# Optimization experiments

Measured on AMD Instinct MI355X. Metric: run time of the kernel, lower is better.

Reference implementation:

```python
import jax, jax.numpy as jnp
import numpy as np

EPS = 1e-5

def conv1x1(x, w):
    # x: (B,C,H,W), w: (O,C) -> (B,O,H,W)
    return jnp.einsum('bchw,oc->bohw', x, w)

def bn_relu(y, g, b, m, v):
    s = g / jnp.sqrt(v + EPS)
    return jax.nn.relu(y * s[None, :, None, None] + (b - m * s)[None, :, None, None])

def cbr(x, w, g, b, m, v):
    return bn_relu(conv1x1(x, w), g, b, m, v)

def _bn_params(key, c):
    k1, k2, k3, k4 = jax.random.split(key, 4)
    g = 1.0 + 0.1 * jax.random.normal(k1, (c,), jnp.float32)
    b = 0.1 * jax.random.normal(k2, (c,), jnp.float32)
    m = 0.05 * jax.random.normal(k3, (c,), jnp.float32)
    v = jax.random.uniform(k4, (c,), jnp.float32, 0.5, 1.5)
    return g, b, m, v

def setup_inputs() -> dict:
    key = jax.random.key(0)
    B, Cin, H, W = 8, 512, 64, 64
    Ck, Cv, Cout = 256, 256, 512
    ks = jax.random.split(key, 12)
    def w(k, o, c):
        return jax.random.normal(k, (o, c), jnp.float32) * (1.0 / np.sqrt(c))
    inp = {}
    inp['x'] = jax.random.normal(ks[0], (B, Cin, H, W), jnp.float32)
    # f_key
    inp['kW1'] = w(ks[1], Ck, Cin); inp['kG1'], inp['kB1'], inp['kM1'], inp['kV1'] = _bn_params(ks[2], Ck)
    inp['kW2'] = w(ks[3], Ck, Ck);  inp['kG2'], inp['kB2'], inp['kM2'], inp['kV2'] = _bn_params(ks[4], Ck)
    # f_query
    inp['qW1'] = w(ks[5], Ck, Cin); inp['qG1'], inp['qB1'], inp['qM1'], inp['qV1'] = _bn_params(ks[6], Ck)
    inp['qW2'] = w(ks[7], Ck, Ck);  inp['qG2'], inp['qB2'], inp['qM2'], inp['qV2'] = _bn_params(ks[8], Ck)
    # f_value
    inp['vW'] = w(ks[9], Cv, Cin)
    # W (output projection)
    inp['wW'] = w(ks[10], Cout, Cv); inp['wG'], inp['wB'], inp['wM'], inp['wV'] = _bn_params(ks[11], Cout)
    return inp

def reference(x,
              kW1, kG1, kB1, kM1, kV1, kW2, kG2, kB2, kM2, kV2,
              qW1, qG1, qB1, qM1, qV1, qW2, qG2, qB2, qM2, qV2,
              vW,
              wW, wG, wB, wM, wV):
    B, _, H, W = x.shape
    q = cbr(cbr(x, qW1, qG1, qB1, qM1, qV1), qW2, qG2, qB2, qM2, qV2)  # (B,Ck,H,W)
    k = cbr(cbr(x, kW1, kG1, kB1, kM1, kV1), kW2, kG2, kB2, kM2, kV2)  # (B,Ck,H,W)
    v = conv1x1(x, vW)                                                  # (B,Cv,H,W)
    Ck = q.shape[1]; Cv = v.shape[1]; N = H * W
    qf = q.reshape(B, Ck, N)   # query = qf^T -> (B,N,Ck)
    kf = k.reshape(B, Ck, N)
    vf = v.reshape(B, Cv, N)
    sim = jnp.einsum('bcn,bcm->bnm', qf, kf) * (Ck ** -0.5)  # (B,N,N)
    attn = jax.nn.softmax(sim, axis=-1)
    ctx = jnp.einsum('bnm,bcm->bcn', attn, vf).reshape(B, Cv, H, W)
    return cbr(ctx, wW, wG, wB, wM, wV)
```

## Files before the change

kernel.cpp:

```cpp
#include <hip/hip_runtime.h>
#include <hip/hip_bf16.h>

typedef __attribute__((ext_vector_type(8))) short bf16x8;
typedef __attribute__((ext_vector_type(4))) float f32x4;

#define MFMA16(a, b, c) __builtin_amdgcn_mfma_f32_16x16x32_bf16(a, b, c, 0, 0, 0)

static __device__ __forceinline__ unsigned short f2bf(float f) {
  union { __hip_bfloat16 h; unsigned short u; } cv;
  cv.h = __float2bfloat16(f);
  return cv.u;
}

static __device__ __forceinline__ void gload16(const void* gptr, void* lptr) {
  __builtin_amdgcn_global_load_lds(
      (const __attribute__((address_space(1))) void*)gptr,
      (__attribute__((address_space(3))) void*)lptr, 16, 0, 0);
}


__global__ void conv_w_k(const float* __restrict__ qW1, const float* __restrict__ kW1,
                         const float* __restrict__ qW2, const float* __restrict__ kW2,
                         const float* __restrict__ vW, const float* __restrict__ wW,
                         __hip_bfloat16* __restrict__ dst) {
  int i = blockIdx.x * 256 + threadIdx.x;
  const float* src; int off;
  if (i < 131072)      { src = qW1; off = i; }
  else if (i < 262144) { src = kW1; off = i - 131072; }
  else if (i < 327680) { src = qW2; off = i - 262144; }
  else if (i < 393216) { src = kW2; off = i - 327680; }
  else if (i < 524288) { src = vW;  off = i - 393216; }
  else                 { src = wW;  off = i - 524288; }
  dst[i] = __float2bfloat16(src[off]);
}

__global__ void bn_all_k(const float* __restrict__ qG1, const float* __restrict__ qB1, const float* __restrict__ qM1, const float* __restrict__ qV1,
                         const float* __restrict__ qG2, const float* __restrict__ qB2, const float* __restrict__ qM2, const float* __restrict__ qV2,
                         const float* __restrict__ kG1, const float* __restrict__ kB1, const float* __restrict__ kM1, const float* __restrict__ kV1,
                         const float* __restrict__ kG2, const float* __restrict__ kB2, const float* __restrict__ kM2, const float* __restrict__ kV2,
                         const float* __restrict__ wG, const float* __restrict__ wB, const float* __restrict__ wM, const float* __restrict__ wV,
                         float* __restrict__ base) {
  int bidx = blockIdx.x, tid = threadIdx.x;
  const float *g, *b, *m, *v; float *s, *t; int i;
  if (bidx == 0)      { g = qG1; b = qB1; m = qM1; v = qV1; s = base;        t = base + 256;  i = tid; }
  else if (bidx == 1) { g = qG2; b = qB2; m = qM2; v = qV2; s = base + 512;  t = base + 768;  i = tid; }
  else if (bidx == 2) { g = kG1; b = kB1; m = kM1; v = kV1; s = base + 1024; t = base + 1280; i = tid; }
  else if (bidx == 3) { g = kG2; b = kB2; m = kM2; v = kV2; s = base + 1536; t = base + 1792; i = tid; }
  else                { g = wG;  b = wB;  m = wM;  v = wV;  s = base + 2048; t = base + 2560; i = (bidx - 4) * 256 + tid; }
  float sv = g[i] * rsqrtf(v[i] + 1e-5f);
  s[i] = sv;
  t[i] = b[i] - m[i] * sv;
}

__global__ __launch_bounds__(256) void transpose_k(const float* __restrict__ x,
                                                   __hip_bfloat16* __restrict__ xT) {
  __shared__ float tile[64][65];
  const int n0 = blockIdx.x * 64, c0 = blockIdx.y * 64, b = blockIdx.z;
  const int tx = threadIdx.x, ty = threadIdx.y;
  const float* xp = x + ((size_t)(b * 512 + c0) * 4096) + n0;
#pragma unroll
  for (int i = 0; i < 16; ++i) {
    int c = ty + 4 * i;
    tile[c][tx] = xp[(size_t)c * 4096 + tx];
  }
  __syncthreads();
  __hip_bfloat16* op = xT + ((size_t)(b * 4096 + n0) * 512) + c0;
#pragma unroll
  for (int i = 0; i < 16; ++i) {
    int nl = ty + 4 * i;
    op[(size_t)nl * 512 + tx] = __float2bfloat16(tile[tx][nl]);
  }
}

template <int EPI>
__global__ __launch_bounds__(256) void gemm_nt_k(
    const __hip_bfloat16* __restrict__ A, long sA,
    const __hip_bfloat16* __restrict__ B, long sB,
    void* __restrict__ Cp, long sC,
    int lda, int ldb, int ldc, int K,
    const float* __restrict__ s, const float* __restrict__ t) {
  __shared__ short As[128][72];
  __shared__ short Bs[128][72];
  const int tid = threadIdx.x;
  const int w = tid >> 6, l = tid & 63, g = l >> 4, ln = l & 15;
  const int wr = w >> 1, wc = w & 1;
  const int rb = blockIdx.x * 128, cb = blockIdx.y * 128;
  const __hip_bfloat16* Ab = A + (size_t)blockIdx.z * sA;
  const __hip_bfloat16* Bb = B + (size_t)blockIdx.z * sB;

  f32x4 acc[4][4];
#pragma unroll
  for (int i = 0; i < 4; ++i)
#pragma unroll
    for (int j = 0; j < 4; ++j) acc[i][j] = (f32x4){0.f, 0.f, 0.f, 0.f};

  const int r0 = tid >> 3;
  const int c8 = (tid & 7) * 8;

  for (int k0 = 0; k0 < K; k0 += 64) {
#pragma unroll
    for (int i = 0; i < 4; ++i) {
      const int r = r0 + 32 * i;
      *(uint4*)&As[r][c8] = *(const uint4*)(Ab + (size_t)(rb + r) * lda + (k0 + c8));
      *(uint4*)&Bs[r][c8] = *(const uint4*)(Bb + (size_t)(cb + r) * ldb + (k0 + c8));
    }
    __syncthreads();
#pragma unroll
    for (int kk = 0; kk < 2; ++kk) {
      bf16x8 av[4], bv[4];
#pragma unroll
      for (int i = 0; i < 4; ++i) av[i] = *(const bf16x8*)&As[64 * wr + 16 * i + ln][32 * kk + 8 * g];
#pragma unroll
      for (int i = 0; i < 4; ++i) bv[i] = *(const bf16x8*)&Bs[64 * wc + 16 * i + ln][32 * kk + 8 * g];
#pragma unroll
      for (int mi = 0; mi < 4; ++mi)
#pragma unroll
        for (int ni = 0; ni < 4; ++ni)
          acc[mi][ni] = MFMA16(av[mi], bv[ni], acc[mi][ni]);
    }
    __syncthreads();
  }

  const int row0 = rb + 64 * wr + 4 * g;
  const int col0 = cb + 64 * wc + ln;

  if (EPI == 2) {
    float* C = (float*)Cp + (size_t)blockIdx.z * sC;
#pragma unroll
    for (int mi = 0; mi < 4; ++mi) {
#pragma unroll
      for (int r = 0; r < 4; ++r) {
        const int R = row0 + 16 * mi + r;
        const float sr = s[R], tr = t[R];
#pragma unroll
        for (int ni = 0; ni < 4; ++ni) {
          float v = fmaf(acc[mi][ni][r], sr, tr);
          C[(size_t)R * ldc + (col0 + 16 * ni)] = v > 0.f ? v : 0.f;
        }
      }
    }
  } else {
    __hip_bfloat16* C = (__hip_bfloat16*)Cp + (size_t)blockIdx.z * sC;
    float sc[4], tc[4];
    if (EPI == 1) {
#pragma unroll
      for (int ni = 0; ni < 4; ++ni) { sc[ni] = s[col0 + 16 * ni]; tc[ni] = t[col0 + 16 * ni]; }
    }
#pragma unroll
    for (int mi = 0; mi < 4; ++mi) {
#pragma unroll
      for (int ni = 0; ni < 4; ++ni) {
#pragma unroll
        for (int r = 0; r < 4; ++r) {
          float v = acc[mi][ni][r];
          if (EPI == 1) { v = fmaf(v, sc[ni], tc[ni]); v = v > 0.f ? v : 0.f; }
          C[(size_t)(row0 + 16 * mi + r) * ldc + (col0 + 16 * ni)] = __float2bfloat16(v);
        }
      }
    }
  }
}

__global__ __launch_bounds__(256, 2) void flash_k(
    const __hip_bfloat16* __restrict__ Q,
    const __hip_bfloat16* __restrict__ Kt,
    const __hip_bfloat16* __restrict__ V,
    __hip_bfloat16* __restrict__ O) {
  __shared__ short Ks[64 * 256];
  __shared__ short Ps[64 * 64];
  __shared__ float aLds[64];
  __shared__ float lLds[64];
  __shared__ int fLds[4];

  const int tid = threadIdx.x;
  const int w = tid >> 6, l = tid & 63, g = l >> 4, ln = l & 15;
  const int bid = blockIdx.x;
  const int batch = bid & 7;
  const int qb = (bid >> 3) << 6;
  const size_t bo = (size_t)batch * (4096 * 256);
  const float CE = 0.09016844005556021f;

  const int swz45 = (16 * g) ^ ((ln & 3) << 4);
  const int s6 = ((ln >> 2) & 1) << 6;
  const char* Ks0 = (const char*)Ks + (ln * 512 + swz45 + s6);
  const char* Ks1 = Ks0 + (((ln >> 2) & 1) ? -64 : 64);
  const char* Pr0 = (const char*)Ps + (ln * 128 + swz45 + s6);
  const char* Pr1 = Pr0 + (((ln >> 2) & 1) ? -64 : 64);
  const int pwOff = (16 * w + ln) * 128 + 8 * (g & 1) + (((g >> 1) ^ (ln & 1)) << 4) +
                    (((ln >> 1) & 1) << 5) + s6;

  bf16x8 qf[8];
  {
    const __hip_bfloat16* qp = Q + bo + (size_t)(qb + 16 * w + ln) * 256 + 8 * g;
#pragma unroll
    for (int kk = 0; kk < 8; ++kk) qf[kk] = *(const bf16x8*)(qp + 32 * kk);
  }

  f32x4 acc[4][4];
#pragma unroll
  for (int qg = 0; qg < 4; ++qg)
#pragma unroll
    for (int ci = 0; ci < 4; ++ci) acc[qg][ci] = (f32x4){0.f, 0.f, 0.f, 0.f};
  float m_run = -1e30f, l_run = 0.f;

  const int kRow = 16 * w + (l >> 5);
  const int kChunk = (l & 31) ^ (l >> 5);
  const short* Kb = (const short*)(Kt + bo);
  const short* Vp = (const short*)(V + bo) + (size_t)(64 * w + ln) * 4096 + 8 * g;

  auto stageK = [&](int m0) {
#pragma unroll
    for (int j = 0; j < 8; ++j) {
      const short* gp = Kb + (size_t)(m0 + kRow + 2 * j) * 256 + 8 * (kChunk ^ ((2 * j) & 7));
      gload16(gp, Ks + w * 4096 + j * 512);
    }
  };

  stageK(0);
  __builtin_amdgcn_sched_barrier(0);

  for (int t = 0; t < 64; ++t) {
    const int m0 = t << 6;

    bf16x8 vfr[8];
#pragma unroll
    for (int ci = 0; ci < 4; ++ci)
#pragma unroll
      for (int kk = 0; kk < 2; ++kk) {
        const short* gp = Vp + (size_t)ci * (16 * 4096) + (m0 + 32 * kk);
        asm volatile("global_load_dwordx4 %0, %1, off" : "=v"(vfr[2 * ci + kk]) : "v"(gp));
      }
    __builtin_amdgcn_sched_barrier(0);

    asm volatile("s_waitcnt vmcnt(8)" ::: "memory");
    __builtin_amdgcn_sched_barrier(0);
    __builtin_amdgcn_s_barrier();
    asm volatile("" ::: "memory");
    __builtin_amdgcn_sched_barrier(0);

    f32x4 sf[4];
#pragma unroll
    for (int mi = 0; mi < 4; ++mi) sf[mi] = (f32x4){0.f, 0.f, 0.f, 0.f};
    __builtin_amdgcn_s_setprio(1);
#pragma unroll
    for (int kk = 0; kk < 8; ++kk) {
      const char* kp = ((kk & 1) ? Ks1 : Ks0) + 128 * (kk >> 1);
#pragma unroll
      for (int mi = 0; mi < 4; ++mi) {
        bf16x8 a = *(const bf16x8*)(kp + 8192 * mi);
        sf[mi] = MFMA16(a, qf[kk], sf[mi]);
      }
    }
    __builtin_amdgcn_s_setprio(0);

    float sv[16];
#pragma unroll
    for (int mi = 0; mi < 4; ++mi)
#pragma unroll
      for (int r = 0; r < 4; ++r) sv[4 * mi + r] = sf[mi][r];
    float a0 = fmaxf(fmaxf(sv[0], sv[1]), sv[2]);
    float a1 = fmaxf(fmaxf(sv[3], sv[4]), sv[5]);
    float a2 = fmaxf(fmaxf(sv[6], sv[7]), sv[8]);
    float a3 = fmaxf(fmaxf(sv[9], sv[10]), sv[11]);
    float a4 = fmaxf(fmaxf(sv[12], sv[13]), sv[14]);
    float mmax = fmaxf(fmaxf(fmaxf(fmaxf(a0, a1), a2), fmaxf(a3, a4)), sv[15]);
    mmax = fmaxf(mmax, __shfl_xor(mmax, 16));
    mmax = fmaxf(mmax, __shfl_xor(mmax, 32));

    float alpha = 1.0f;
    int rs = 0;
    if (!__all((mmax - m_run) * CE <= 8.0f)) {
      float m_new = fmaxf(m_run, mmax);
      alpha = exp2f((m_run - m_new) * CE);
      l_run *= alpha;
      m_run = m_new;
      rs = 1;
    }
    float p[16], psum = 0.f;
#pragma unroll
    for (int j = 0; j < 16; ++j) {
      p[j] = exp2f((sv[j] - m_run) * CE);
      psum += p[j];
    }
    psum += __shfl_xor(psum, 16);
    psum += __shfl_xor(psum, 32);
    l_run += psum;

    {
      uint2 pk0, pk1, pk2, pk3;
      pk0.x = (unsigned int)f2bf(p[0])  | ((unsigned int)f2bf(p[1])  << 16);
      pk0.y = (unsigned int)f2bf(p[2])  | ((unsigned int)f2bf(p[3])  << 16);
      pk1.x = (unsigned int)f2bf(p[4])  | ((unsigned int)f2bf(p[5])  << 16);
      pk1.y = (unsigned int)f2bf(p[6])  | ((unsigned int)f2bf(p[7])  << 16);
      pk2.x = (unsigned int)f2bf(p[8])  | ((unsigned int)f2bf(p[9])  << 16);
      pk2.y = (unsigned int)f2bf(p[10]) | ((unsigned int)f2bf(p[11]) << 16);
      pk3.x = (unsigned int)f2bf(p[12]) | ((unsigned int)f2bf(p[13]) << 16);
      pk3.y = (unsigned int)f2bf(p[14]) | ((unsigned int)f2bf(p[15]) << 16);
      char* Pb = (char*)Ps;
      *(uint2*)(Pb + (pwOff ^ 0))  = pk0;
      *(uint2*)(Pb + (pwOff ^ 32)) = pk1;
      *(uint2*)(Pb + (pwOff ^ 64)) = pk2;
      *(uint2*)(Pb + (pwOff ^ 96)) = pk3;
    }
    if (g == 0) aLds[16 * w + ln] = alpha;
    if (l == 0) fLds[w] = rs;

    asm volatile("" ::: "memory");
    __builtin_amdgcn_sched_barrier(0);
    __builtin_amdgcn_s_barrier();
    asm volatile("" ::: "memory");
    __builtin_amdgcn_sched_barrier(0);

    if (t < 63) stageK(m0 + 64);
    __builtin_amdgcn_sched_barrier(0);

    {
      int4 fl = *(const int4*)fLds;
      if (fl.x | fl.y | fl.z | fl.w) {
#pragma unroll
        for (int qg = 0; qg < 4; ++qg) {
          f32x4 av = *(const f32x4*)&aLds[16 * qg + 4 * g];
#pragma unroll
          for (int ci = 0; ci < 4; ++ci) acc[qg][ci] *= av;
        }
      }
    }

    if (t < 63) {
      asm volatile("s_waitcnt vmcnt(8)" ::: "memory");
    } else {
      asm volatile("s_waitcnt vmcnt(0)" ::: "memory");
    }
    __builtin_amdgcn_sched_barrier(0);

    __builtin_amdgcn_s_setprio(1);
#pragma unroll
    for (int kk = 0; kk < 2; ++kk) {
#pragma unroll
      for (int qg = 0; qg < 4; ++qg) {
        bf16x8 pa = *(const bf16x8*)((kk ? Pr1 : Pr0) + 2048 * qg);
#pragma unroll
        for (int ci = 0; ci < 4; ++ci)
          acc[qg][ci] = MFMA16(pa, vfr[2 * ci + kk], acc[qg][ci]);
      }
    }
    __builtin_amdgcn_s_setprio(0);
    __builtin_amdgcn_sched_barrier(0);
  }

  if (g == 0) lLds[16 * w + ln] = l_run;
  asm volatile("" ::: "memory");
  __builtin_amdgcn_s_barrier();
  asm volatile("" ::: "memory");

  __hip_bfloat16* Ob = O + bo;
#pragma unroll
  for (int qg = 0; qg < 4; ++qg) {
    f32x4 lv = *(const f32x4*)&lLds[16 * qg + 4 * g];
    f32x4 li;
#pragma unroll
    for (int r = 0; r < 4; ++r) li[r] = 1.0f / lv[r];
#pragma unroll
    for (int ci = 0; ci < 4; ++ci) {
#pragma unroll
      for (int r = 0; r < 4; ++r) {
        float val = acc[qg][ci][r] * li[r];
        Ob[(size_t)(qb + 16 * qg + 4 * g + r) * 256 + 64 * w + 16 * ci + ln] = __float2bfloat16(val);
      }
    }
  }
}


extern "C" void kernel_launch(void* const* d_in, const int* in_sizes, int n_in,
                              void* d_out, int out_size, void* d_ws, size_t ws_size,
                              hipStream_t stream) {
  const float* x   = (const float*)d_in[0];
  const float* kW1 = (const float*)d_in[1];
  const float* kG1 = (const float*)d_in[2];
  const float* kB1 = (const float*)d_in[3];
  const float* kM1 = (const float*)d_in[4];
  const float* kV1 = (const float*)d_in[5];
  const float* kW2 = (const float*)d_in[6];
  const float* kG2 = (const float*)d_in[7];
  const float* kB2 = (const float*)d_in[8];
  const float* kM2 = (const float*)d_in[9];
  const float* kV2 = (const float*)d_in[10];
  const float* qW1 = (const float*)d_in[11];
  const float* qG1 = (const float*)d_in[12];
  const float* qB1 = (const float*)d_in[13];
  const float* qM1 = (const float*)d_in[14];
  const float* qV1 = (const float*)d_in[15];
  const float* qW2 = (const float*)d_in[16];
  const float* qG2 = (const float*)d_in[17];
  const float* qB2 = (const float*)d_in[18];
  const float* qM2 = (const float*)d_in[19];
  const float* qV2 = (const float*)d_in[20];
  const float* vW  = (const float*)d_in[21];
  const float* wW  = (const float*)d_in[22];
  const float* wG  = (const float*)d_in[23];
  const float* wB  = (const float*)d_in[24];
  const float* wM  = (const float*)d_in[25];
  const float* wV  = (const float*)d_in[26];

  char* ws = (char*)d_ws;
  __hip_bfloat16* bQW1 = (__hip_bfloat16*)(ws + 0);
  __hip_bfloat16* bKW1 = (__hip_bfloat16*)(ws + 262144);
  __hip_bfloat16* bQW2 = (__hip_bfloat16*)(ws + 524288);
  __hip_bfloat16* bKW2 = (__hip_bfloat16*)(ws + 655360);
  __hip_bfloat16* bVW  = (__hip_bfloat16*)(ws + 786432);
  __hip_bfloat16* bWW  = (__hip_bfloat16*)(ws + 1048576);
  float* bnBase = (float*)(ws + 1310720);
  float* sQ1 = bnBase + 0;
  float* tQ1 = bnBase + 256;
  float* sQ2 = bnBase + 512;
  float* tQ2 = bnBase + 768;
  float* sK1 = bnBase + 1024;
  float* tK1 = bnBase + 1280;
  float* sK2 = bnBase + 1536;
  float* tK2 = bnBase + 1792;
  float* sWo = bnBase + 2048;
  float* tWo = bnBase + 2560;
  __hip_bfloat16* xT   = (__hip_bfloat16*)(ws + 2097152);
  __hip_bfloat16* bufA = (__hip_bfloat16*)(ws + 35651584);
  __hip_bfloat16* q2b  = (__hip_bfloat16*)(ws + 52428800);
  __hip_bfloat16* k2b  = (__hip_bfloat16*)(ws + 69206016);
  __hip_bfloat16* vB   = (__hip_bfloat16*)(ws + 85983232);

  conv_w_k<<<2560, 256, 0, stream>>>(qW1, kW1, qW2, kW2, vW, wW, bQW1);
  bn_all_k<<<6, 256, 0, stream>>>(qG1, qB1, qM1, qV1, qG2, qB2, qM2, qV2,
                                  kG1, kB1, kM1, kV1, kG2, kB2, kM2, kV2,
                                  wG, wB, wM, wV, bnBase);

  transpose_k<<<dim3(64, 8, 8), dim3(64, 4), 0, stream>>>(x, xT);

  gemm_nt_k<1><<<dim3(32, 2, 8), 256, 0, stream>>>(xT, 2097152L, bQW1, 0L, bufA, 1048576L,
                                                   512, 512, 256, 512, sQ1, tQ1);
  gemm_nt_k<1><<<dim3(32, 2, 8), 256, 0, stream>>>(bufA, 1048576L, bQW2, 0L, q2b, 1048576L,
                                                   256, 256, 256, 256, sQ2, tQ2);
  gemm_nt_k<1><<<dim3(32, 2, 8), 256, 0, stream>>>(xT, 2097152L, bKW1, 0L, bufA, 1048576L,
                                                   512, 512, 256, 512, sK1, tK1);
  gemm_nt_k<1><<<dim3(32, 2, 8), 256, 0, stream>>>(bufA, 1048576L, bKW2, 0L, k2b, 1048576L,
                                                   256, 256, 256, 256, sK2, tK2);
  gemm_nt_k<0><<<dim3(2, 32, 8), 256, 0, stream>>>(bVW, 0L, xT, 2097152L, vB, 1048576L,
                                                   512, 512, 4096, 512, nullptr, nullptr);
  flash_k<<<512, 256, 0, stream>>>(q2b, k2b, vB, bufA);
  gemm_nt_k<2><<<dim3(4, 32, 8), 256, 0, stream>>>(bWW, 0L, bufA, 1048576L, d_out, 2097152L,
                                                   256, 256, 4096, 256, sWo, tWo);
}
```

Measured before the change: 308.4 us.

## Split attention KV range across two blocks and merge partial results

The flash attention kernel now splits the key/value sequence into two halves, one per block, doubling the grid from 512 to 1024 blocks. A new merge kernel then combines the two partial outputs using per-row scale and sum arrays. The online max rescaling is also dropped: each block fixes its max from its first tile and clamps the exponent, which removes the alpha rescale and its LDS traffic. The cost is an extra kernel launch, extra partial-output memory traffic, and a numerical risk if later tiles exceed the first tile's max by a large margin.

```diff
diff --git a/kernel.cpp b/kernel.cpp
--- a/kernel.cpp
+++ b/kernel.cpp
@@ -10,6 +10,12 @@
   union { __hip_bfloat16 h; unsigned short u; } cv;
   cv.h = __float2bfloat16(f);
   return cv.u;
+}
+
+static __device__ __forceinline__ float bf2f(short s) {
+  union { float f; unsigned u; } cv;
+  cv.u = ((unsigned)(unsigned short)s) << 16;
+  return cv.f;
 }
 
 static __device__ __forceinline__ void gload16(const void* gptr, void* lptr) {
@@ -165,18 +171,19 @@
     const __hip_bfloat16* __restrict__ Q,
     const __hip_bfloat16* __restrict__ Kt,
     const __hip_bfloat16* __restrict__ V,
-    __hip_bfloat16* __restrict__ O) {
+    __hip_bfloat16* __restrict__ part,
+    float* __restrict__ cArr,
+    float* __restrict__ lArr) {
   __shared__ short Ks[64 * 256];
   __shared__ short Ps[64 * 64];
-  __shared__ float aLds[64];
-  __shared__ float lLds[64];
-  __shared__ int fLds[4];
 
   const int tid = threadIdx.x;
   const int w = tid >> 6, l = tid & 63, g = l >> 4, ln = l & 15;
   const int bid = blockIdx.x;
   const int batch = bid & 7;
-  const int qb = (bid >> 3) << 6;
+  const int half = (bid >> 3) & 1;
+  const int qb = (bid >> 4) << 6;
+  const int kvBase = half << 11;
   const size_t bo = (size_t)batch * (4096 * 256);
   const float CE = 0.09016844005556021f;
 
@@ -201,26 +208,30 @@
   for (int qg = 0; qg < 4; ++qg)
 #pragma unroll
     for (int ci = 0; ci < 4; ++ci) acc[qg][ci] = (f32x4){0.f, 0.f, 0.f, 0.f};
-  float m_run = -1e30f, l_run = 0.f;
+  float l_run = 0.f;
+  float cval = 0.f;
 
   const int kRow = 16 * w + (l >> 5);
   const int kChunk = (l & 31) ^ (l >> 5);
   const short* Kb = (const short*)(Kt + bo);
   const short* Vp = (const short*)(V + bo) + (size_t)(64 * w + ln) * 4096 + 8 * g;
 
-  auto stageK = [&](int m0) {
-#pragma unroll
-    for (int j = 0; j < 8; ++j) {
-      const short* gp = Kb + (size_t)(m0 + kRow + 2 * j) * 256 + 8 * (kChunk ^ ((2 * j) & 7));
-      gload16(gp, Ks + w * 4096 + j * 512);
-    }
-  };
-
-  stageK(0);
-  __builtin_amdgcn_sched_barrier(0);
-
-  for (int t = 0; t < 64; ++t) {
-    const int m0 = t << 6;
+#define SB __builtin_amdgcn_sched_barrier(0)
+
+#define STAGEK(M0)                                                             \
+  do {                                                                         \
+    _Pragma("unroll") for (int j = 0; j < 8; ++j) {                            \
+      const short* gp =                                                        \
+          Kb + (size_t)((M0) + kRow + 2 * j) * 256 + 8 * (kChunk ^ ((2 * j) & 7)); \
+      gload16(gp, Ks + w * 4096 + j * 512);                                    \
+    }                                                                          \
+  } while (0)
+
+  STAGEK(kvBase);
+  SB;
+
+  for (int t = 0; t < 32; ++t) {
+    const int m0 = kvBase + (t << 6);
 
     bf16x8 vfr[8];
 #pragma unroll
@@ -228,15 +239,16 @@
 #pragma unroll
       for (int kk = 0; kk < 2; ++kk) {
         const short* gp = Vp + (size_t)ci * (16 * 4096) + (m0 + 32 * kk);
-        asm volatile("global_load_dwordx4 %0, %1, off" : "=v"(vfr[2 * ci + kk]) : "v"(gp));
-      }
-    __builtin_amdgcn_sched_barrier(0);
+        asm volatile("global_load_dwordx4 %0, %1, off"
+                     : "=v"(vfr[2 * ci + kk]) : "v"(gp));
+      }
+    SB;
 
     asm volatile("s_waitcnt vmcnt(8)" ::: "memory");
-    __builtin_amdgcn_sched_barrier(0);
+    SB;
     __builtin_amdgcn_s_barrier();
     asm volatile("" ::: "memory");
-    __builtin_amdgcn_sched_barrier(0);
+    SB;
 
     f32x4 sf[4];
 #pragma unroll
@@ -258,28 +270,21 @@
     for (int mi = 0; mi < 4; ++mi)
 #pragma unroll
       for (int r = 0; r < 4; ++r) sv[4 * mi + r] = sf[mi][r];
-    float a0 = fmaxf(fmaxf(sv[0], sv[1]), sv[2]);
-    float a1 = fmaxf(fmaxf(sv[3], sv[4]), sv[5]);
-    float a2 = fmaxf(fmaxf(sv[6], sv[7]), sv[8]);
-    float a3 = fmaxf(fmaxf(sv[9], sv[10]), sv[11]);
-    float a4 = fmaxf(fmaxf(sv[12], sv[13]), sv[14]);
-    float mmax = fmaxf(fmaxf(fmaxf(fmaxf(a0, a1), a2), fmaxf(a3, a4)), sv[15]);
-    mmax = fmaxf(mmax, __shfl_xor(mmax, 16));
-    mmax = fmaxf(mmax, __shfl_xor(mmax, 32));
-
-    float alpha = 1.0f;
-    int rs = 0;
-    if (!__all((mmax - m_run) * CE <= 8.0f)) {
-      float m_new = fmaxf(m_run, mmax);
-      alpha = exp2f((m_run - m_new) * CE);
-      l_run *= alpha;
-      m_run = m_new;
-      rs = 1;
+    if (t == 0) {
+      float a0 = fmaxf(fmaxf(sv[0], sv[1]), sv[2]);
+      float a1 = fmaxf(fmaxf(sv[3], sv[4]), sv[5]);
+      float a2 = fmaxf(fmaxf(sv[6], sv[7]), sv[8]);
+      float a3 = fmaxf(fmaxf(sv[9], sv[10]), sv[11]);
+      float a4 = fmaxf(fmaxf(sv[12], sv[13]), sv[14]);
+      float mmax = fmaxf(fmaxf(fmaxf(fmaxf(a0, a1), a2), fmaxf(a3, a4)), sv[15]);
+      mmax = fmaxf(mmax, __shfl_xor(mmax, 16));
+      mmax = fmaxf(mmax, __shfl_xor(mmax, 32));
+      cval = mmax * CE;
     }
     float p[16], psum = 0.f;
 #pragma unroll
     for (int j = 0; j < 16; ++j) {
-      p[j] = exp2f((sv[j] - m_run) * CE);
+      p[j] = exp2f(fminf(fmaf(sv[j], CE, -cval), 63.0f));
       psum += p[j];
     }
     psum += __shfl_xor(psum, 16);
@@ -288,50 +293,35 @@
 
     {
       uint2 pk0, pk1, pk2, pk3;
-      pk0.x = (unsigned int)f2bf(p[0])  | ((unsigned int)f2bf(p[1])  << 16);
-      pk0.y = (unsigned int)f2bf(p[2])  | ((unsigned int)f2bf(p[3])  << 16);
-      pk1.x = (unsigned int)f2bf(p[4])  | ((unsigned int)f2bf(p[5])  << 16);
-      pk1.y = (unsigned int)f2bf(p[6])  | ((unsigned int)f2bf(p[7])  << 16);
-      pk2.x = (unsigned int)f2bf(p[8])  | ((unsigned int)f2bf(p[9])  << 16);
-      pk2.y = (unsigned int)f2bf(p[10]) | ((unsigned int)f2bf(p[11]) << 16);
-      pk3.x = (unsigned int)f2bf(p[12]) | ((unsigned int)f2bf(p[13]) << 16);
-      pk3.y = (unsigned int)f2bf(p[14]) | ((unsigned int)f2bf(p[15]) << 16);
+      pk0.x = (unsigned)f2bf(p[0])  | ((unsigned)f2bf(p[1])  << 16);
+      pk0.y = (unsigned)f2bf(p[2])  | ((unsigned)f2bf(p[3])  << 16);
+      pk1.x = (unsigned)f2bf(p[4])  | ((unsigned)f2bf(p[5])  << 16);
+      pk1.y = (unsigned)f2bf(p[6])  | ((unsigned)f2bf(p[7])  << 16);
+      pk2.x = (unsigned)f2bf(p[8])  | ((unsigned)f2bf(p[9])  << 16);
+      pk2.y = (unsigned)f2bf(p[10]) | ((unsigned)f2bf(p[11]) << 16);
+      pk3.x = (unsigned)f2bf(p[12]) | ((unsigned)f2bf(p[13]) << 16);
+      pk3.y = (unsigned)f2bf(p[14]) | ((unsigned)f2bf(p[15]) << 16);
       char* Pb = (char*)Ps;
       *(uint2*)(Pb + (pwOff ^ 0))  = pk0;
       *(uint2*)(Pb + (pwOff ^ 32)) = pk1;
       *(uint2*)(Pb + (pwOff ^ 64)) = pk2;
       *(uint2*)(Pb + (pwOff ^ 96)) = pk3;
     }
-    if (g == 0) aLds[16 * w + ln] = alpha;
-    if (l == 0) fLds[w] = rs;
-
-    asm volatile("" ::: "memory");
-    __builtin_amdgcn_sched_barrier(0);
+
+    asm volatile("s_waitcnt lgkmcnt(0)" ::: "memory");
+    SB;
     __builtin_amdgcn_s_barrier();
     asm volatile("" ::: "memory");
-    __builtin_amdgcn_sched_barrier(0);
-
-    if (t < 63) stageK(m0 + 64);
-    __builtin_amdgcn_sched_barrier(0);
-
-    {
-      int4 fl = *(const int4*)fLds;
-      if (fl.x | fl.y | fl.z | fl.w) {
-#pragma unroll
-        for (int qg = 0; qg < 4; ++qg) {
-          f32x4 av = *(const f32x4*)&aLds[16 * qg + 4 * g];
-#pragma unroll
-          for (int ci = 0; ci < 4; ++ci) acc[qg][ci] *= av;
-        }
-      }
-    }
-
-    if (t < 63) {
+    SB;
+
+    if (t < 31) {
+      STAGEK(m0 + 64);
+      SB;
       asm volatile("s_waitcnt vmcnt(8)" ::: "memory");
     } else {
       asm volatile("s_waitcnt vmcnt(0)" ::: "memory");
     }
-    __builtin_amdgcn_sched_barrier(0);
+    SB;
 
     __builtin_amdgcn_s_setprio(1);
 #pragma unroll
@@ -345,18 +335,25 @@
       }
     }
     __builtin_amdgcn_s_setprio(0);
-    __builtin_amdgcn_sched_barrier(0);
-  }
-
-  if (g == 0) lLds[16 * w + ln] = l_run;
-  asm volatile("" ::: "memory");
-  __builtin_amdgcn_s_barrier();
-  asm volatile("" ::: "memory");
-
-  __hip_bfloat16* Ob = O + bo;
+    SB;
+  }
+#undef STAGEK
+#undef SB
+
+  __syncthreads();
+  float* Pf = (float*)Ps;
+  if (g == 0) {
+    Pf[16 * w + ln] = l_run;
+    const int qi = (half * 8 + batch) * 4096 + qb + 16 * w + ln;
+    cArr[qi] = cval;
+    lArr[qi] = l_run;
+  }
+  __syncthreads();
+
+  __hip_bfloat16* pb = part + ((size_t)(half * 8 + batch) * 4096 + qb) * 256;
 #pragma unroll
   for (int qg = 0; qg < 4; ++qg) {
-    f32x4 lv = *(const f32x4*)&lLds[16 * qg + 4 * g];
+    f32x4 lv = *(const f32x4*)&Pf[16 * qg + 4 * g];
     f32x4 li;
 #pragma unroll
     for (int r = 0; r < 4; ++r) li[r] = 1.0f / lv[r];
@@ -365,10 +362,40 @@
 #pragma unroll
       for (int r = 0; r < 4; ++r) {
         float val = acc[qg][ci][r] * li[r];
-        Ob[(size_t)(qb + 16 * qg + 4 * g + r) * 256 + 64 * w + 16 * ci + ln] = __float2bfloat16(val);
-      }
-    }
-  }
+        pb[(size_t)(16 * qg + 4 * g + r) * 256 + 64 * w + 16 * ci + ln] = __float2bfloat16(val);
+      }
+    }
+  }
+}
+
+__global__ __launch_bounds__(256) void merge_k(
+    const __hip_bfloat16* __restrict__ part,
+    const float* __restrict__ cArr, const float* __restrict__ lArr,
+    __hip_bfloat16* __restrict__ ctx) {
+  const int tid = threadIdx.x;
+  const int R = blockIdx.x * 8 + (tid >> 5);
+  const int cv = (tid & 31) * 8;
+  const float c0 = cArr[R], c1 = cArr[32768 + R];
+  const float l0 = lArr[R], l1 = lArr[32768 + R];
+  const float Cm = fmaxf(c0, c1);
+  float w0 = (l0 > 0.f) ? exp2f(c0 - Cm) * l0 : 0.f;
+  float w1 = (l1 > 0.f) ? exp2f(c1 - Cm) * l1 : 0.f;
+  const float sum = w0 + w1;
+  const float inv = sum > 0.f ? 1.0f / sum : 0.f;
+  w0 *= inv;
+  w1 *= inv;
+  const short* p0 = (const short*)part + (size_t)R * 256 + cv;
+  const short* p1 = p0 + (size_t)32768 * 256;
+  bf16x8 a0 = *(const bf16x8*)p0;
+  bf16x8 a1 = *(const bf16x8*)p1;
+  bf16x8 o;
+#pragma unroll
+  for (int j = 0; j < 8; ++j) {
+    float v0 = (w0 > 0.f) ? w0 * bf2f(a0[j]) : 0.f;
+    float v1 = (w1 > 0.f) ? w1 * bf2f(a1[j]) : 0.f;
+    o[j] = (short)f2bf(v0 + v1);
+  }
+  *(bf16x8*)((short*)ctx + (size_t)R * 256 + cv) = o;
 }
 
 
@@ -421,6 +448,8 @@
   float* tK2 = bnBase + 1792;
   float* sWo = bnBase + 2048;
   float* tWo = bnBase + 2560;
+  float* cArr = (float*)(ws + 1572864);
+  float* lArr = (float*)(ws + 1835008);
   __hip_bfloat16* xT   = (__hip_bfloat16*)(ws + 2097152);
   __hip_bfloat16* bufA = (__hip_bfloat16*)(ws + 35651584);
   __hip_bfloat16* q2b  = (__hip_bfloat16*)(ws + 52428800);
@@ -444,7 +473,8 @@
                                                    256, 256, 256, 256, sK2, tK2);
   gemm_nt_k<0><<<dim3(2, 32, 8), 256, 0, stream>>>(bVW, 0L, xT, 2097152L, vB, 1048576L,
                                                    512, 512, 4096, 512, nullptr, nullptr);
-  flash_k<<<512, 256, 0, stream>>>(q2b, k2b, vB, bufA);
+  flash_k<<<1024, 256, 0, stream>>>(q2b, k2b, vB, xT, cArr, lArr);
+  merge_k<<<4096, 256, 0, stream>>>(xT, cArr, lArr, bufA);
   gemm_nt_k<2><<<dim3(4, 32, 8), 256, 0, stream>>>(bWW, 0L, bufA, 1048576L, d_out, 2097152L,
                                                    256, 256, 4096, 256, sWo, tWo);
 }
```

Measured after the change: 303.9 us. No clear change (-1.5%).
